# Optimization experiments

Hardware: AMD Instinct MI355X
Metric: run time of the kernel (lower is better)

Reference implementation:

```python
import jax, jax.numpy as jnp
import numpy as np

T, H, I, E, Z, TOPK = 1024, 1024, 512, 32, 8, 4
ROUTED_SCALING = 1.0


def setup_inputs() -> dict:
    key = jax.random.key(0)
    k1, k2, k3, k4 = jax.random.split(key, 4)
    return {
        "hidden_states": jax.random.normal(k1, (T, H), jnp.float32),
        "router_w": jax.random.normal(k2, (E + Z, H), jnp.float32) * 0.02,
        "correction_bias": jnp.zeros((E + Z,), jnp.float32),
        "w_gate_up": jax.random.normal(k3, (E, 2 * I, H), jnp.float32) * 0.02,
        "w_down": jax.random.normal(k4, (E, H, I), jnp.float32) * 0.02,
        "top_k": TOPK,
    }


def reference(hidden_states, router_w, correction_bias, w_gate_up, w_down, top_k):
    # hidden_states: [T, H]; router_w: [E+Z, H]; w_gate_up: [E, 2I, H]; w_down: [E, H, I]
    t, h = hidden_states.shape
    e = w_gate_up.shape[0]
    i = w_down.shape[2]
    # --- router (float32, no bias; correction bias only affects selection) ---
    logits = jnp.einsum("th,eh->te", hidden_states.astype(jnp.float32), router_w)
    scores = jax.nn.softmax(logits, axis=-1)                     # [T, E+Z]
    _, idx = jax.lax.top_k(scores + correction_bias[None, :], top_k)  # [T, k]
    w = jnp.take_along_axis(scores, idx, axis=1) * ROUTED_SCALING     # renormalize=False
    # combine matrix [T, E+Z] (sparse top-k scattered dense)
    comb = jnp.zeros((t, scores.shape[1]), jnp.float32)
    comb = comb.at[jnp.arange(t)[:, None], idx].add(w)
    comb_routed = comb[:, :e].astype(hidden_states.dtype)        # [T, E]
    zero_w = comb[:, e:].sum(-1).astype(hidden_states.dtype)     # [T] identity zero-experts
    # --- grouped SiLU-gated expert MLPs (dense all-experts reference) ---
    gu = jnp.einsum("th,eih->eti", hidden_states, w_gate_up)     # [E, T, 2I]
    hmid = jax.nn.silu(gu[..., :i]) * gu[..., i:]                # [E, T, I]
    ye = jnp.einsum("eti,ehi->eth", hmid, w_down)                # [E, T, H]
    out = jnp.einsum("te,eth->th", comb_routed, ye)
    out = out + zero_w[:, None] * hidden_states
    return out
```

## Files before the change

### kernel.cpp

```cpp
#include <hip/hip_runtime.h>
#include <hip/hip_cooperative_groups.h>
#include <hip/hip_bf16.h>
#include <math.h>

namespace cg = cooperative_groups;

#define TT   1024
#define HH   1024
#define II   512
#define EE   32
#define NE   40
#define TOPK 4
#define CAP  1024

#define GM  128
#define GNP 32
#define GK  32
#define KP  40
#define DN  64

typedef __attribute__((ext_vector_type(4))) short short4v;
typedef __attribute__((ext_vector_type(8))) short short8v;
typedef __attribute__((ext_vector_type(4))) float floatx4;

static __device__ __forceinline__ short f2bf(float f) {
    unsigned u = __float_as_uint(f);
    unsigned r = (u + 0x7fffu + ((u >> 16) & 1u)) >> 16;
    return (short)(r & 0xffffu);
}
static __device__ __forceinline__ float bf2f(short s) {
    return __uint_as_float(((unsigned)(unsigned short)s) << 16);
}
#if defined(__has_builtin)
#if __has_builtin(__builtin_amdgcn_cvt_pk_bf16_f32)
#define HAVE_PK_BF16 1
#endif
#endif
static __device__ __forceinline__ unsigned pk2(float a, float b) {
#ifdef HAVE_PK_BF16
    typedef __attribute__((ext_vector_type(2))) __bf16 bf2t;
    union { bf2t v; unsigned u; } cv;
    cv.v = __builtin_amdgcn_cvt_pk_bf16_f32(a, b);
    return cv.u;
#else
    return (unsigned)(unsigned short)f2bf(a) | ((unsigned)(unsigned short)f2bf(b) << 16);
#endif
}
static __device__ __forceinline__ short4v cvt4(float4 v) {
    union { unsigned u[2]; short4v s; } cv;
    cv.u[0] = pk2(v.x, v.y); cv.u[1] = pk2(v.z, v.w);
    return cv.s;
}

struct SMem {
    short As[GM * KP];
    short Bs[2 * GNP * KP];
    int   sl[GM];
    float wvs[GM];
};


static __device__ __forceinline__ void phaseA(
    const int bx, const int tid,
    const float* __restrict__ x, const float* __restrict__ rw,
    const float* __restrict__ bias,
    float* __restrict__ topk_w, float* __restrict__ zero_w,
    int* __restrict__ kexp, int* __restrict__ counts,
    int* __restrict__ slots, short* __restrict__ xb)
{
    const int lane = tid & 63;
    const int w    = tid >> 6;

    if (w < 2) {
        const int t = bx * 2 + w;
        float xv[16];
        #pragma unroll
        for (int i = 0; i < 16; ++i) xv[i] = x[(size_t)t * HH + 64 * i + lane];

        float mylogit = -INFINITY;
        for (int e0 = 0; e0 < NE; e0 += 4) {
            const float* r0 = rw + (size_t)e0 * HH;
            float p[4] = { 0.f, 0.f, 0.f, 0.f };
            #pragma unroll
            for (int i = 0; i < 16; ++i) {
                int h = 64 * i + lane;
                #pragma unroll
                for (int j = 0; j < 4; ++j) p[j] += xv[i] * r0[(size_t)j * HH + h];
            }
            #pragma unroll
            for (int j = 0; j < 4; ++j) {
                #pragma unroll
                for (int off = 32; off > 0; off >>= 1) p[j] += __shfl_xor(p[j], off);
                if (lane == e0 + j) mylogit = p[j];
            }
        }

        float m = mylogit;
        #pragma unroll
        for (int off = 32; off > 0; off >>= 1) m = fmaxf(m, __shfl_xor(m, off));
        float pexp = (lane < NE) ? expf(mylogit - m) : 0.f;
        float s = pexp;
        #pragma unroll
        for (int off = 32; off > 0; off >>= 1) s += __shfl_xor(s, off);
        const float score = pexp / s;

        float val = (lane < NE) ? score + bias[lane] : -INFINITY;
        int   kidx[TOPK];
        float kw[TOPK];
        #pragma unroll
        for (int k = 0; k < TOPK; ++k) {
            float v = val; int idx = lane;
            #pragma unroll
            for (int off = 32; off > 0; off >>= 1) {
                float ov = __shfl_xor(v, off);
                int   oi = __shfl_xor(idx, off);
                if (ov > v || (ov == v && oi < idx)) { v = ov; idx = oi; }
            }
            kidx[k] = idx;
            kw[k]   = __shfl(score, idx);
            if (lane == idx) val = -INFINITY;
        }

        if (lane == 0) {
            float zw = 0.f;
            #pragma unroll
            for (int k = 0; k < TOPK; ++k) {
                int slot = t * TOPK + k;
                topk_w[slot] = kw[k];
                kexp[slot]   = kidx[k];
                if (kidx[k] < EE) {
                    int pos = atomicAdd(&counts[kidx[k]], 1);
                    slots[kidx[k] * CAP + pos] = slot;
                } else {
                    zw += kw[k];
                }
            }
            zero_w[t] = zw;
        }
    } else {
        const int t = bx * 2 + (w - 2);
        const float4* xr = (const float4*)(x + (size_t)t * HH);
        short4v* xbr = (short4v*)(xb + (size_t)t * HH);
        #pragma unroll
        for (int i = 0; i < 4; ++i) xbr[lane + 64 * i] = cvt4(xr[lane + 64 * i]);
    }
}

static __device__ __forceinline__ void phaseB(
    const int bx, const int tid, SMem* sm,
    const short* __restrict__ xb, const float* __restrict__ wgu,
    const int* __restrict__ counts, const int* __restrict__ slots,
    const float* __restrict__ topk_w, short* __restrict__ hmid)
{
    const int e      = bx >> 4;
    const int c_base = (bx & 15) * GNP;
    const int cnt    = counts[e];
    const float* wb  = wgu + (size_t)e * (2 * II) * HH;

    const int lane = tid & 63;
    const int w    = tid >> 6;
    const int wy   = w & 1;
    const int wx   = w >> 1;
    const int quad = lane >> 4;
    const int mcol = lane & 15;

    for (int m_base = 0; m_base < cnt; m_base += GM) {
        if (tid < GM) {
            int m = m_base + tid;
            int s = (m < cnt) ? slots[e * CAP + m] : -1;
            sm->sl[tid]  = s;
            sm->wvs[tid] = (s >= 0) ? topk_w[s] : 0.f;
        }
        __syncthreads();

        const int kcA = tid & 3;
        int rowA[2]; int slA[2]; const short* pA[2];
        #pragma unroll
        for (int it = 0; it < 2; ++it) {
            rowA[it] = (tid >> 2) + 64 * it;
            int s = sm->sl[rowA[it]];
            slA[it] = s;
            pA[it] = xb + (size_t)((s >= 0 ? s : 0) >> 2) * HH + kcA * 8;
        }
        const int kq = tid & 7;
        int rowB[2]; const float* pB[2];
        #pragma unroll
        for (int it = 0; it < 2; ++it) {
            rowB[it] = (tid >> 3) + 32 * it;
            int grow = (rowB[it] < GNP) ? (c_base + rowB[it])
                                        : (II + c_base + rowB[it] - GNP);
            pB[it] = wb + (size_t)grow * HH + kq * 4;
        }

        floatx4 accg[4] = {};
        floatx4 accu[4] = {};
        short8v pa[2]; float4 pb[2];
        const short8v szv = { 0,0,0,0,0,0,0,0 };

        #pragma unroll
        for (int it = 0; it < 2; ++it) pa[it] = (slA[it] >= 0) ? *(const short8v*)(pA[it]) : szv;
        #pragma unroll
        for (int it = 0; it < 2; ++it) pb[it] = *(const float4*)(pB[it]);

        for (int k0 = 0; k0 < HH; k0 += GK) {
            #pragma unroll
            for (int it = 0; it < 2; ++it) *(short8v*)&sm->As[rowA[it] * KP + kcA * 8] = pa[it];
            #pragma unroll
            for (int it = 0; it < 2; ++it) *(short4v*)&sm->Bs[rowB[it] * KP + kq * 4] = cvt4(pb[it]);
            __syncthreads();

            const int kn = k0 + GK;
            if (kn < HH) {
                #pragma unroll
                for (int it = 0; it < 2; ++it) pa[it] = (slA[it] >= 0) ? *(const short8v*)(pA[it] + kn) : szv;
                #pragma unroll
                for (int it = 0; it < 2; ++it) pb[it] = *(const float4*)(pB[it] + kn);
            }

            short8v a[4], bg, bu;
            #pragma unroll
            for (int i = 0; i < 4; ++i)
                a[i] = *(const short8v*)&sm->As[(wy * 64 + i * 16 + mcol) * KP + quad * 8];
            bg = *(const short8v*)&sm->Bs[(wx * 16 + mcol) * KP + quad * 8];
            bu = *(const short8v*)&sm->Bs[(GNP + wx * 16 + mcol) * KP + quad * 8];
            #pragma unroll
            for (int i = 0; i < 4; ++i) {
                accg[i] = __builtin_amdgcn_mfma_f32_16x16x32_bf16(a[i], bg, accg[i], 0, 0, 0);
                accu[i] = __builtin_amdgcn_mfma_f32_16x16x32_bf16(a[i], bu, accu[i], 0, 0, 0);
            }
            __syncthreads();
        }

        #pragma unroll
        for (int i = 0; i < 4; ++i) {
            #pragma unroll
            for (int r = 0; r < 4; ++r) {
                int m = wy * 64 + i * 16 + quad * 4 + r;
                int s = sm->sl[m];
                if (s < 0) continue;
                float g = accg[i][r], u = accu[i][r];
                float valf = sm->wvs[m] * g * u / (1.f + __expf(-g));
                hmid[(size_t)s * II + c_base + wx * 16 + mcol] = f2bf(valf);
            }
        }
        __syncthreads();
    }
}

static __device__ __forceinline__ void phaseC(
    const int bx, const int tid, SMem* sm,
    const short* __restrict__ hmid, const float* __restrict__ wd,
    const int* __restrict__ counts, const int* __restrict__ slots,
    short* __restrict__ ydown)
{
    const int e      = bx >> 4;
    const int n_base = (bx & 15) * DN;
    const int cnt    = counts[e];
    const float* wb  = wd + (size_t)e * HH * II;

    const int lane = tid & 63;
    const int w    = tid >> 6;
    const int wy   = w & 1;
    const int wx   = w >> 1;
    const int quad = lane >> 4;
    const int mcol = lane & 15;

    for (int m_base = 0; m_base < cnt; m_base += GM) {
        if (tid < GM) {
            int m = m_base + tid;
            sm->sl[tid] = (m < cnt) ? slots[e * CAP + m] : -1;
        }
        __syncthreads();

        const int kcA = tid & 3;
        int rowA[2]; int slA[2]; const short* pA[2];
        #pragma unroll
        for (int it = 0; it < 2; ++it) {
            rowA[it] = (tid >> 2) + 64 * it;
            int s = sm->sl[rowA[it]];
            slA[it] = s;
            pA[it] = hmid + (size_t)(s >= 0 ? s : 0) * II + kcA * 8;
        }
        const int kq = tid & 7;
        int rowB[2]; const float* pB[2];
        #pragma unroll
        for (int it = 0; it < 2; ++it) {
            rowB[it] = (tid >> 3) + 32 * it;
            pB[it] = wb + (size_t)(n_base + rowB[it]) * II + kq * 4;
        }

        floatx4 acc[4][2] = {};
        short8v pa[2]; float4 pb[2];
        const short8v szv = { 0,0,0,0,0,0,0,0 };

        #pragma unroll
        for (int it = 0; it < 2; ++it) pa[it] = (slA[it] >= 0) ? *(const short8v*)(pA[it]) : szv;
        #pragma unroll
        for (int it = 0; it < 2; ++it) pb[it] = *(const float4*)(pB[it]);

        for (int k0 = 0; k0 < II; k0 += GK) {
            #pragma unroll
            for (int it = 0; it < 2; ++it) *(short8v*)&sm->As[rowA[it] * KP + kcA * 8] = pa[it];
            #pragma unroll
            for (int it = 0; it < 2; ++it) *(short4v*)&sm->Bs[rowB[it] * KP + kq * 4] = cvt4(pb[it]);
            __syncthreads();

            const int kn = k0 + GK;
            if (kn < II) {
                #pragma unroll
                for (int it = 0; it < 2; ++it) pa[it] = (slA[it] >= 0) ? *(const short8v*)(pA[it] + kn) : szv;
                #pragma unroll
                for (int it = 0; it < 2; ++it) pb[it] = *(const float4*)(pB[it] + kn);
            }

            short8v a[4], b[2];
            #pragma unroll
            for (int i = 0; i < 4; ++i)
                a[i] = *(const short8v*)&sm->As[(wy * 64 + i * 16 + mcol) * KP + quad * 8];
            #pragma unroll
            for (int j = 0; j < 2; ++j)
                b[j] = *(const short8v*)&sm->Bs[(wx * 32 + j * 16 + mcol) * KP + quad * 8];
            #pragma unroll
            for (int i = 0; i < 4; ++i)
                #pragma unroll
                for (int j = 0; j < 2; ++j)
                    acc[i][j] = __builtin_amdgcn_mfma_f32_16x16x32_bf16(a[i], b[j], acc[i][j], 0, 0, 0);
            __syncthreads();
        }

        #pragma unroll
        for (int i = 0; i < 4; ++i) {
            #pragma unroll
            for (int r = 0; r < 4; ++r) {
                int m = wy * 64 + i * 16 + quad * 4 + r;
                int s = sm->sl[m];
                if (s < 0) continue;
                short* yrow = ydown + (size_t)s * HH + n_base + wx * 32;
                #pragma unroll
                for (int j = 0; j < 2; ++j)
                    yrow[j * 16 + mcol] = f2bf(acc[i][j][r]);
            }
        }
        __syncthreads();
    }
}

static __device__ __forceinline__ void phaseD(
    const int bx, const int tid,
    const float* __restrict__ x, const short* __restrict__ ydown,
    const int* __restrict__ kexp, const float* __restrict__ zero_w,
    float* __restrict__ out)
{
    #pragma unroll
    for (int j = 0; j < 2; ++j) {
        const int t = bx * 2 + j;
        const float4 xvv = ((const float4*)(x + (size_t)t * HH))[tid];
        const float zw = zero_w[t];
        float4 o;
        o.x = zw * xvv.x; o.y = zw * xvv.y; o.z = zw * xvv.z; o.w = zw * xvv.w;
        #pragma unroll
        for (int k = 0; k < TOPK; ++k) {
            int slot = t * TOPK + k;
            if (kexp[slot] < EE) {
                short4v y = *(const short4v*)&ydown[(size_t)slot * HH + tid * 4];
                o.x += bf2f(y[0]); o.y += bf2f(y[1]);
                o.z += bf2f(y[2]); o.w += bf2f(y[3]);
            }
        }
        ((float4*)(out + (size_t)t * HH))[tid] = o;
    }
}

__global__ __launch_bounds__(256, 2) void fused_moe(
    const float* __restrict__ x, const float* __restrict__ rw,
    const float* __restrict__ bias, const float* __restrict__ wgu,
    const float* __restrict__ wd, float* __restrict__ out,
    int* __restrict__ counts, float* __restrict__ topk_w,
    float* __restrict__ zero_w, int* __restrict__ kexp,
    int* __restrict__ slots, short* __restrict__ xb,
    short* __restrict__ hmid, short* __restrict__ ydown)
{
    cg::grid_group grid = cg::this_grid();
    __shared__ SMem sm;
    const int bx = blockIdx.x, tid = threadIdx.x;

    phaseA(bx, tid, x, rw, bias, topk_w, zero_w, kexp, counts, slots, xb);
    __threadfence(); grid.sync();
    phaseB(bx, tid, &sm, xb, wgu, counts, slots, topk_w, hmid);
    __threadfence(); grid.sync();
    phaseC(bx, tid, &sm, hmid, wd, counts, slots, ydown);
    __threadfence(); grid.sync();
    phaseD(bx, tid, x, ydown, kexp, zero_w, out);
}

__global__ __launch_bounds__(256, 2) void kA(
    const float* __restrict__ x, const float* __restrict__ rw,
    const float* __restrict__ bias, float* __restrict__ topk_w,
    float* __restrict__ zero_w, int* __restrict__ kexp,
    int* __restrict__ counts, int* __restrict__ slots, short* __restrict__ xb)
{
    phaseA(blockIdx.x, threadIdx.x, x, rw, bias, topk_w, zero_w, kexp, counts, slots, xb);
}
__global__ __launch_bounds__(256, 2) void kB(
    const short* __restrict__ xb, const float* __restrict__ wgu,
    const int* __restrict__ counts, const int* __restrict__ slots,
    const float* __restrict__ topk_w, short* __restrict__ hmid)
{
    __shared__ SMem sm;
    phaseB(blockIdx.x, threadIdx.x, &sm, xb, wgu, counts, slots, topk_w, hmid);
}
__global__ __launch_bounds__(256, 2) void kC(
    const short* __restrict__ hmid, const float* __restrict__ wd,
    const int* __restrict__ counts, const int* __restrict__ slots,
    short* __restrict__ ydown)
{
    __shared__ SMem sm;
    phaseC(blockIdx.x, threadIdx.x, &sm, hmid, wd, counts, slots, ydown);
}
__global__ __launch_bounds__(256, 2) void kD(
    const float* __restrict__ x, const short* __restrict__ ydown,
    const int* __restrict__ kexp, const float* __restrict__ zero_w,
    float* __restrict__ out)
{
    phaseD(blockIdx.x, threadIdx.x, x, ydown, kexp, zero_w, out);
}

extern "C" void kernel_launch(void* const* d_in, const int* in_sizes, int n_in,
                              void* d_out, int out_size, void* d_ws, size_t ws_size,
                              hipStream_t stream) {
    const float* x    = (const float*)d_in[0];
    const float* rw   = (const float*)d_in[1];
    const float* bias = (const float*)d_in[2];
    const float* wgu  = (const float*)d_in[3];
    const float* wd   = (const float*)d_in[4];
    float* out = (float*)d_out;

    char* ws = (char*)d_ws;
    int*   counts = (int*)ws;
    float* topk_w = (float*)(ws + 1024);
    float* zero_w = (float*)(ws + 17408);
    int*   kexp   = (int*)(ws + 21504);
    int*   slots  = (int*)(ws + 40960);
    short* xb     = (short*)(ws + 262144);
    short* hmid   = (short*)(ws + 2359296);
    short* ydown  = (short*)(ws + 6553600);

    hipMemsetAsync(counts, 0, EE * sizeof(int), stream);

    int nb = 0;
    hipError_t qerr = hipOccupancyMaxActiveBlocksPerMultiprocessor(&nb, fused_moe, 256, 0);
    bool launched = false;
    if (qerr == hipSuccess && nb >= 2) {
        void* args[] = {
            (void*)&x, (void*)&rw, (void*)&bias, (void*)&wgu, (void*)&wd,
            (void*)&out, (void*)&counts, (void*)&topk_w, (void*)&zero_w,
            (void*)&kexp, (void*)&slots, (void*)&xb, (void*)&hmid, (void*)&ydown
        };
        hipError_t lerr = hipLaunchCooperativeKernel((const void*)fused_moe,
                                                     dim3(512), dim3(256),
                                                     args, 0, stream);
        launched = (lerr == hipSuccess);
    }
    if (!launched) {
        kA<<<dim3(512), dim3(256), 0, stream>>>(x, rw, bias, topk_w, zero_w, kexp, counts, slots, xb);
        kB<<<dim3(512), dim3(256), 0, stream>>>(xb, wgu, counts, slots, topk_w, hmid);
        kC<<<dim3(512), dim3(256), 0, stream>>>(hmid, wd, counts, slots, ydown);
        kD<<<dim3(512), dim3(256), 0, stream>>>(x, ydown, kexp, zero_w, out);
    }
}
```

Before: 311.7 us.

## Replace cooperative fused kernel with four launches using smaller tiles

Removes the cooperative single-kernel path with grid syncs and always launches four separate kernels. Tile widths for the gate/up and down GEMMs are halved so each expert gets 32 blocks, giving 1024 blocks per GEMM, and each warp now owns 32 rows. Launch bounds rise to 4 blocks per CU and the combine kernel uses one block per token. The aim is more parallelism and occupancy and no grid-wide barriers, at the cost of extra launch overhead and more redundant reads of the activation rows per expert.

```diff
diff --git a/kernel.cpp b/kernel.cpp
--- a/kernel.cpp
+++ b/kernel.cpp
@@ -1,9 +1,6 @@
 #include <hip/hip_runtime.h>
-#include <hip/hip_cooperative_groups.h>
 #include <hip/hip_bf16.h>
 #include <math.h>
-
-namespace cg = cooperative_groups;
 
 #define TT   1024
 #define HH   1024
@@ -14,10 +11,10 @@
 #define CAP  1024
 
 #define GM  128
-#define GNP 32
+#define GNP 16
 #define GK  32
 #define KP  40
-#define DN  64
+#define DN  32
 
 typedef __attribute__((ext_vector_type(4))) short short4v;
 typedef __attribute__((ext_vector_type(8))) short short8v;
@@ -60,14 +57,13 @@
 };
 
 
-static __device__ __forceinline__ void phaseA(
-    const int bx, const int tid,
+__global__ __launch_bounds__(256, 4) void kA(
     const float* __restrict__ x, const float* __restrict__ rw,
-    const float* __restrict__ bias,
-    float* __restrict__ topk_w, float* __restrict__ zero_w,
-    int* __restrict__ kexp, int* __restrict__ counts,
-    int* __restrict__ slots, short* __restrict__ xb)
+    const float* __restrict__ bias, float* __restrict__ topk_w,
+    float* __restrict__ zero_w, int* __restrict__ kexp,
+    int* __restrict__ counts, int* __restrict__ slots, short* __restrict__ xb)
 {
+    const int bx = blockIdx.x, tid = threadIdx.x;
     const int lane = tid & 63;
     const int w    = tid >> 6;
 
@@ -146,283 +142,210 @@
     }
 }
 
-static __device__ __forceinline__ void phaseB(
-    const int bx, const int tid, SMem* sm,
-    const short* __restrict__ xb, const float* __restrict__ wgu,
-    const int* __restrict__ counts, const int* __restrict__ slots,
-    const float* __restrict__ topk_w, short* __restrict__ hmid)
-{
-    const int e      = bx >> 4;
-    const int c_base = (bx & 15) * GNP;
-    const int cnt    = counts[e];
-    const float* wb  = wgu + (size_t)e * (2 * II) * HH;
-
-    const int lane = tid & 63;
-    const int w    = tid >> 6;
-    const int wy   = w & 1;
-    const int wx   = w >> 1;
-    const int quad = lane >> 4;
-    const int mcol = lane & 15;
-
-    for (int m_base = 0; m_base < cnt; m_base += GM) {
-        if (tid < GM) {
-            int m = m_base + tid;
-            int s = (m < cnt) ? slots[e * CAP + m] : -1;
-            sm->sl[tid]  = s;
-            sm->wvs[tid] = (s >= 0) ? topk_w[s] : 0.f;
-        }
-        __syncthreads();
-
-        const int kcA = tid & 3;
-        int rowA[2]; int slA[2]; const short* pA[2];
-        #pragma unroll
-        for (int it = 0; it < 2; ++it) {
-            rowA[it] = (tid >> 2) + 64 * it;
-            int s = sm->sl[rowA[it]];
-            slA[it] = s;
-            pA[it] = xb + (size_t)((s >= 0 ? s : 0) >> 2) * HH + kcA * 8;
-        }
-        const int kq = tid & 7;
-        int rowB[2]; const float* pB[2];
-        #pragma unroll
-        for (int it = 0; it < 2; ++it) {
-            rowB[it] = (tid >> 3) + 32 * it;
-            int grow = (rowB[it] < GNP) ? (c_base + rowB[it])
-                                        : (II + c_base + rowB[it] - GNP);
-            pB[it] = wb + (size_t)grow * HH + kq * 4;
-        }
-
-        floatx4 accg[4] = {};
-        floatx4 accu[4] = {};
-        short8v pa[2]; float4 pb[2];
-        const short8v szv = { 0,0,0,0,0,0,0,0 };
-
-        #pragma unroll
-        for (int it = 0; it < 2; ++it) pa[it] = (slA[it] >= 0) ? *(const short8v*)(pA[it]) : szv;
-        #pragma unroll
-        for (int it = 0; it < 2; ++it) pb[it] = *(const float4*)(pB[it]);
-
-        for (int k0 = 0; k0 < HH; k0 += GK) {
-            #pragma unroll
-            for (int it = 0; it < 2; ++it) *(short8v*)&sm->As[rowA[it] * KP + kcA * 8] = pa[it];
-            #pragma unroll
-            for (int it = 0; it < 2; ++it) *(short4v*)&sm->Bs[rowB[it] * KP + kq * 4] = cvt4(pb[it]);
-            __syncthreads();
-
-            const int kn = k0 + GK;
-            if (kn < HH) {
-                #pragma unroll
-                for (int it = 0; it < 2; ++it) pa[it] = (slA[it] >= 0) ? *(const short8v*)(pA[it] + kn) : szv;
-                #pragma unroll
-                for (int it = 0; it < 2; ++it) pb[it] = *(const float4*)(pB[it] + kn);
-            }
-
-            short8v a[4], bg, bu;
-            #pragma unroll
-            for (int i = 0; i < 4; ++i)
-                a[i] = *(const short8v*)&sm->As[(wy * 64 + i * 16 + mcol) * KP + quad * 8];
-            bg = *(const short8v*)&sm->Bs[(wx * 16 + mcol) * KP + quad * 8];
-            bu = *(const short8v*)&sm->Bs[(GNP + wx * 16 + mcol) * KP + quad * 8];
-            #pragma unroll
-            for (int i = 0; i < 4; ++i) {
-                accg[i] = __builtin_amdgcn_mfma_f32_16x16x32_bf16(a[i], bg, accg[i], 0, 0, 0);
-                accu[i] = __builtin_amdgcn_mfma_f32_16x16x32_bf16(a[i], bu, accu[i], 0, 0, 0);
-            }
-            __syncthreads();
-        }
-
-        #pragma unroll
-        for (int i = 0; i < 4; ++i) {
-            #pragma unroll
-            for (int r = 0; r < 4; ++r) {
-                int m = wy * 64 + i * 16 + quad * 4 + r;
-                int s = sm->sl[m];
-                if (s < 0) continue;
-                float g = accg[i][r], u = accu[i][r];
-                float valf = sm->wvs[m] * g * u / (1.f + __expf(-g));
-                hmid[(size_t)s * II + c_base + wx * 16 + mcol] = f2bf(valf);
-            }
-        }
-        __syncthreads();
-    }
-}
-
-static __device__ __forceinline__ void phaseC(
-    const int bx, const int tid, SMem* sm,
-    const short* __restrict__ hmid, const float* __restrict__ wd,
-    const int* __restrict__ counts, const int* __restrict__ slots,
-    short* __restrict__ ydown)
-{
-    const int e      = bx >> 4;
-    const int n_base = (bx & 15) * DN;
-    const int cnt    = counts[e];
-    const float* wb  = wd + (size_t)e * HH * II;
-
-    const int lane = tid & 63;
-    const int w    = tid >> 6;
-    const int wy   = w & 1;
-    const int wx   = w >> 1;
-    const int quad = lane >> 4;
-    const int mcol = lane & 15;
-
-    for (int m_base = 0; m_base < cnt; m_base += GM) {
-        if (tid < GM) {
-            int m = m_base + tid;
-            sm->sl[tid] = (m < cnt) ? slots[e * CAP + m] : -1;
-        }
-        __syncthreads();
-
-        const int kcA = tid & 3;
-        int rowA[2]; int slA[2]; const short* pA[2];
-        #pragma unroll
-        for (int it = 0; it < 2; ++it) {
-            rowA[it] = (tid >> 2) + 64 * it;
-            int s = sm->sl[rowA[it]];
-            slA[it] = s;
-            pA[it] = hmid + (size_t)(s >= 0 ? s : 0) * II + kcA * 8;
-        }
-        const int kq = tid & 7;
-        int rowB[2]; const float* pB[2];
-        #pragma unroll
-        for (int it = 0; it < 2; ++it) {
-            rowB[it] = (tid >> 3) + 32 * it;
-            pB[it] = wb + (size_t)(n_base + rowB[it]) * II + kq * 4;
-        }
-
-        floatx4 acc[4][2] = {};
-        short8v pa[2]; float4 pb[2];
-        const short8v szv = { 0,0,0,0,0,0,0,0 };
-
-        #pragma unroll
-        for (int it = 0; it < 2; ++it) pa[it] = (slA[it] >= 0) ? *(const short8v*)(pA[it]) : szv;
-        #pragma unroll
-        for (int it = 0; it < 2; ++it) pb[it] = *(const float4*)(pB[it]);
-
-        for (int k0 = 0; k0 < II; k0 += GK) {
-            #pragma unroll
-            for (int it = 0; it < 2; ++it) *(short8v*)&sm->As[rowA[it] * KP + kcA * 8] = pa[it];
-            #pragma unroll
-            for (int it = 0; it < 2; ++it) *(short4v*)&sm->Bs[rowB[it] * KP + kq * 4] = cvt4(pb[it]);
-            __syncthreads();
-
-            const int kn = k0 + GK;
-            if (kn < II) {
-                #pragma unroll
-                for (int it = 0; it < 2; ++it) pa[it] = (slA[it] >= 0) ? *(const short8v*)(pA[it] + kn) : szv;
-                #pragma unroll
-                for (int it = 0; it < 2; ++it) pb[it] = *(const float4*)(pB[it] + kn);
-            }
-
-            short8v a[4], b[2];
-            #pragma unroll
-            for (int i = 0; i < 4; ++i)
-                a[i] = *(const short8v*)&sm->As[(wy * 64 + i * 16 + mcol) * KP + quad * 8];
-            #pragma unroll
-            for (int j = 0; j < 2; ++j)
-                b[j] = *(const short8v*)&sm->Bs[(wx * 32 + j * 16 + mcol) * KP + quad * 8];
-            #pragma unroll
-            for (int i = 0; i < 4; ++i)
-                #pragma unroll
-                for (int j = 0; j < 2; ++j)
-                    acc[i][j] = __builtin_amdgcn_mfma_f32_16x16x32_bf16(a[i], b[j], acc[i][j], 0, 0, 0);
-            __syncthreads();
-        }
-
-        #pragma unroll
-        for (int i = 0; i < 4; ++i) {
-            #pragma unroll
-            for (int r = 0; r < 4; ++r) {
-                int m = wy * 64 + i * 16 + quad * 4 + r;
-                int s = sm->sl[m];
-                if (s < 0) continue;
-                short* yrow = ydown + (size_t)s * HH + n_base + wx * 32;
-                #pragma unroll
-                for (int j = 0; j < 2; ++j)
-                    yrow[j * 16 + mcol] = f2bf(acc[i][j][r]);
-            }
-        }
-        __syncthreads();
-    }
-}
-
-static __device__ __forceinline__ void phaseD(
-    const int bx, const int tid,
-    const float* __restrict__ x, const short* __restrict__ ydown,
-    const int* __restrict__ kexp, const float* __restrict__ zero_w,
-    float* __restrict__ out)
-{
-    #pragma unroll
-    for (int j = 0; j < 2; ++j) {
-        const int t = bx * 2 + j;
-        const float4 xvv = ((const float4*)(x + (size_t)t * HH))[tid];
-        const float zw = zero_w[t];
-        float4 o;
-        o.x = zw * xvv.x; o.y = zw * xvv.y; o.z = zw * xvv.z; o.w = zw * xvv.w;
-        #pragma unroll
-        for (int k = 0; k < TOPK; ++k) {
-            int slot = t * TOPK + k;
-            if (kexp[slot] < EE) {
-                short4v y = *(const short4v*)&ydown[(size_t)slot * HH + tid * 4];
-                o.x += bf2f(y[0]); o.y += bf2f(y[1]);
-                o.z += bf2f(y[2]); o.w += bf2f(y[3]);
-            }
-        }
-        ((float4*)(out + (size_t)t * HH))[tid] = o;
-    }
-}
-
-__global__ __launch_bounds__(256, 2) void fused_moe(
-    const float* __restrict__ x, const float* __restrict__ rw,
-    const float* __restrict__ bias, const float* __restrict__ wgu,
-    const float* __restrict__ wd, float* __restrict__ out,
-    int* __restrict__ counts, float* __restrict__ topk_w,
-    float* __restrict__ zero_w, int* __restrict__ kexp,
-    int* __restrict__ slots, short* __restrict__ xb,
-    short* __restrict__ hmid, short* __restrict__ ydown)
-{
-    cg::grid_group grid = cg::this_grid();
-    __shared__ SMem sm;
-    const int bx = blockIdx.x, tid = threadIdx.x;
-
-    phaseA(bx, tid, x, rw, bias, topk_w, zero_w, kexp, counts, slots, xb);
-    __threadfence(); grid.sync();
-    phaseB(bx, tid, &sm, xb, wgu, counts, slots, topk_w, hmid);
-    __threadfence(); grid.sync();
-    phaseC(bx, tid, &sm, hmid, wd, counts, slots, ydown);
-    __threadfence(); grid.sync();
-    phaseD(bx, tid, x, ydown, kexp, zero_w, out);
-}
-
-__global__ __launch_bounds__(256, 2) void kA(
-    const float* __restrict__ x, const float* __restrict__ rw,
-    const float* __restrict__ bias, float* __restrict__ topk_w,
-    float* __restrict__ zero_w, int* __restrict__ kexp,
-    int* __restrict__ counts, int* __restrict__ slots, short* __restrict__ xb)
-{
-    phaseA(blockIdx.x, threadIdx.x, x, rw, bias, topk_w, zero_w, kexp, counts, slots, xb);
-}
-__global__ __launch_bounds__(256, 2) void kB(
+__global__ __launch_bounds__(256, 4) void kB(
     const short* __restrict__ xb, const float* __restrict__ wgu,
     const int* __restrict__ counts, const int* __restrict__ slots,
     const float* __restrict__ topk_w, short* __restrict__ hmid)
 {
     __shared__ SMem sm;
-    phaseB(blockIdx.x, threadIdx.x, &sm, xb, wgu, counts, slots, topk_w, hmid);
-}
-__global__ __launch_bounds__(256, 2) void kC(
+    const int bx = blockIdx.x, tid = threadIdx.x;
+    const int e      = bx >> 5;
+    const int c_base = (bx & 31) * GNP;
+    const int cnt    = counts[e];
+    const float* wb  = wgu + (size_t)e * (2 * II) * HH;
+
+    const int lane = tid & 63;
+    const int w    = tid >> 6;
+    const int quad = lane >> 4;
+    const int mcol = lane & 15;
+
+    for (int m_base = 0; m_base < cnt; m_base += GM) {
+        if (tid < GM) {
+            int m = m_base + tid;
+            int s = (m < cnt) ? slots[e * CAP + m] : -1;
+            sm.sl[tid]  = s;
+            sm.wvs[tid] = (s >= 0) ? topk_w[s] : 0.f;
+        }
+        __syncthreads();
+
+        const int kcA = tid & 3;
+        int rowA[2]; int slA[2]; const short* pA[2];
+        #pragma unroll
+        for (int it = 0; it < 2; ++it) {
+            rowA[it] = (tid >> 2) + 64 * it;
+            int s = sm.sl[rowA[it]];
+            slA[it] = s;
+            pA[it] = xb + (size_t)((s >= 0 ? s : 0) >> 2) * HH + kcA * 8;
+        }
+        const int kq   = tid & 7;
+        const int rowB = tid >> 3;
+        const int grow = (rowB < GNP) ? (c_base + rowB)
+                                      : (II + c_base + (rowB - GNP));
+        const float* pB = wb + (size_t)grow * HH + kq * 4;
+
+        floatx4 accg[2] = {};
+        floatx4 accu[2] = {};
+        short8v pa[2]; float4 pb;
+        const short8v szv = { 0,0,0,0,0,0,0,0 };
+
+        #pragma unroll
+        for (int it = 0; it < 2; ++it) pa[it] = (slA[it] >= 0) ? *(const short8v*)(pA[it]) : szv;
+        pb = *(const float4*)(pB);
+
+        for (int k0 = 0; k0 < HH; k0 += GK) {
+            #pragma unroll
+            for (int it = 0; it < 2; ++it) *(short8v*)&sm.As[rowA[it] * KP + kcA * 8] = pa[it];
+            *(short4v*)&sm.Bs[rowB * KP + kq * 4] = cvt4(pb);
+            __syncthreads();
+
+            const int kn = k0 + GK;
+            if (kn < HH) {
+                #pragma unroll
+                for (int it = 0; it < 2; ++it) pa[it] = (slA[it] >= 0) ? *(const short8v*)(pA[it] + kn) : szv;
+                pb = *(const float4*)(pB + kn);
+            }
+
+            short8v a[2], bg, bu;
+            #pragma unroll
+            for (int i = 0; i < 2; ++i)
+                a[i] = *(const short8v*)&sm.As[(w * 32 + i * 16 + mcol) * KP + quad * 8];
+            bg = *(const short8v*)&sm.Bs[(mcol) * KP + quad * 8];
+            bu = *(const short8v*)&sm.Bs[(GNP + mcol) * KP + quad * 8];
+            #pragma unroll
+            for (int i = 0; i < 2; ++i) {
+                accg[i] = __builtin_amdgcn_mfma_f32_16x16x32_bf16(a[i], bg, accg[i], 0, 0, 0);
+                accu[i] = __builtin_amdgcn_mfma_f32_16x16x32_bf16(a[i], bu, accu[i], 0, 0, 0);
+            }
+            __syncthreads();
+        }
+
+        #pragma unroll
+        for (int i = 0; i < 2; ++i) {
+            #pragma unroll
+            for (int r = 0; r < 4; ++r) {
+                int m = w * 32 + i * 16 + quad * 4 + r;
+                int s = sm.sl[m];
+                if (s < 0) continue;
+                float g = accg[i][r], u = accu[i][r];
+                float valf = sm.wvs[m] * g * u / (1.f + __expf(-g));
+                hmid[(size_t)s * II + c_base + mcol] = f2bf(valf);
+            }
+        }
+        __syncthreads();
+    }
+}
+
+__global__ __launch_bounds__(256, 4) void kC(
     const short* __restrict__ hmid, const float* __restrict__ wd,
     const int* __restrict__ counts, const int* __restrict__ slots,
     short* __restrict__ ydown)
 {
     __shared__ SMem sm;
-    phaseC(blockIdx.x, threadIdx.x, &sm, hmid, wd, counts, slots, ydown);
-}
-__global__ __launch_bounds__(256, 2) void kD(
+    const int bx = blockIdx.x, tid = threadIdx.x;
+    const int e      = bx >> 5;
+    const int n_base = (bx & 31) * DN;
+    const int cnt    = counts[e];
+    const float* wb  = wd + (size_t)e * HH * II;
+
+    const int lane = tid & 63;
+    const int w    = tid >> 6;
+    const int quad = lane >> 4;
+    const int mcol = lane & 15;
+
+    for (int m_base = 0; m_base < cnt; m_base += GM) {
+        if (tid < GM) {
+            int m = m_base + tid;
+            sm.sl[tid] = (m < cnt) ? slots[e * CAP + m] : -1;
+        }
+        __syncthreads();
+
+        const int kcA = tid & 3;
+        int rowA[2]; int slA[2]; const short* pA[2];
+        #pragma unroll
+        for (int it = 0; it < 2; ++it) {
+            rowA[it] = (tid >> 2) + 64 * it;
+            int s = sm.sl[rowA[it]];
+            slA[it] = s;
+            pA[it] = hmid + (size_t)(s >= 0 ? s : 0) * II + kcA * 8;
+        }
+        const int kq   = tid & 7;
+        const int rowB = tid >> 3;
+        const float* pB = wb + (size_t)(n_base + rowB) * II + kq * 4;
+
+        floatx4 acc[2][2] = {};
+        short8v pa[2]; float4 pb;
+        const short8v szv = { 0,0,0,0,0,0,0,0 };
+
+        #pragma unroll
+        for (int it = 0; it < 2; ++it) pa[it] = (slA[it] >= 0) ? *(const short8v*)(pA[it]) : szv;
+        pb = *(const float4*)(pB);
+
+        for (int k0 = 0; k0 < II; k0 += GK) {
+            #pragma unroll
+            for (int it = 0; it < 2; ++it) *(short8v*)&sm.As[rowA[it] * KP + kcA * 8] = pa[it];
+            *(short4v*)&sm.Bs[rowB * KP + kq * 4] = cvt4(pb);
+            __syncthreads();
+
+            const int kn = k0 + GK;
+            if (kn < II) {
+                #pragma unroll
+                for (int it = 0; it < 2; ++it) pa[it] = (slA[it] >= 0) ? *(const short8v*)(pA[it] + kn) : szv;
+                pb = *(const float4*)(pB + kn);
+            }
+
+            short8v a[2], b[2];
+            #pragma unroll
+            for (int i = 0; i < 2; ++i)
+                a[i] = *(const short8v*)&sm.As[(w * 32 + i * 16 + mcol) * KP + quad * 8];
+            #pragma unroll
+            for (int j = 0; j < 2; ++j)
+                b[j] = *(const short8v*)&sm.Bs[(j * 16 + mcol) * KP + quad * 8];
+            #pragma unroll
+            for (int i = 0; i < 2; ++i)
+                #pragma unroll
+                for (int j = 0; j < 2; ++j)
+                    acc[i][j] = __builtin_amdgcn_mfma_f32_16x16x32_bf16(a[i], b[j], acc[i][j], 0, 0, 0);
+            __syncthreads();
+        }
+
+        #pragma unroll
+        for (int i = 0; i < 2; ++i) {
+            #pragma unroll
+            for (int r = 0; r < 4; ++r) {
+                int m = w * 32 + i * 16 + quad * 4 + r;
+                int s = sm.sl[m];
+                if (s < 0) continue;
+                short* yrow = ydown + (size_t)s * HH + n_base;
+                #pragma unroll
+                for (int j = 0; j < 2; ++j)
+                    yrow[j * 16 + mcol] = f2bf(acc[i][j][r]);
+            }
+        }
+        __syncthreads();
+    }
+}
+
+__global__ __launch_bounds__(256, 4) void kD(
     const float* __restrict__ x, const short* __restrict__ ydown,
     const int* __restrict__ kexp, const float* __restrict__ zero_w,
     float* __restrict__ out)
 {
-    phaseD(blockIdx.x, threadIdx.x, x, ydown, kexp, zero_w, out);
+    const int bx = blockIdx.x, tid = threadIdx.x;
+    const int t = bx;
+    const float4 xvv = ((const float4*)(x + (size_t)t * HH))[tid];
+    const float zw = zero_w[t];
+    float4 o;
+    o.x = zw * xvv.x; o.y = zw * xvv.y; o.z = zw * xvv.z; o.w = zw * xvv.w;
+    #pragma unroll
+    for (int k = 0; k < TOPK; ++k) {
+        int slot = t * TOPK + k;
+        if (kexp[slot] < EE) {
+            short4v y = *(const short4v*)&ydown[(size_t)slot * HH + tid * 4];
+            o.x += bf2f(y[0]); o.y += bf2f(y[1]);
+            o.z += bf2f(y[2]); o.w += bf2f(y[3]);
+        }
+    }
+    ((float4*)(out + (size_t)t * HH))[tid] = o;
 }
 
 extern "C" void kernel_launch(void* const* d_in, const int* in_sizes, int n_in,
@@ -447,24 +370,8 @@
 
     hipMemsetAsync(counts, 0, EE * sizeof(int), stream);
 
-    int nb = 0;
-    hipError_t qerr = hipOccupancyMaxActiveBlocksPerMultiprocessor(&nb, fused_moe, 256, 0);
-    bool launched = false;
-    if (qerr == hipSuccess && nb >= 2) {
-        void* args[] = {
-            (void*)&x, (void*)&rw, (void*)&bias, (void*)&wgu, (void*)&wd,
-            (void*)&out, (void*)&counts, (void*)&topk_w, (void*)&zero_w,
-            (void*)&kexp, (void*)&slots, (void*)&xb, (void*)&hmid, (void*)&ydown
-        };
-        hipError_t lerr = hipLaunchCooperativeKernel((const void*)fused_moe,
-                                                     dim3(512), dim3(256),
-                                                     args, 0, stream);
-        launched = (lerr == hipSuccess);
-    }
-    if (!launched) {
-        kA<<<dim3(512), dim3(256), 0, stream>>>(x, rw, bias, topk_w, zero_w, kexp, counts, slots, xb);
-        kB<<<dim3(512), dim3(256), 0, stream>>>(xb, wgu, counts, slots, topk_w, hmid);
-        kC<<<dim3(512), dim3(256), 0, stream>>>(hmid, wd, counts, slots, ydown);
-        kD<<<dim3(512), dim3(256), 0, stream>>>(x, ydown, kexp, zero_w, out);
-    }
-}
+    kA<<<dim3(512),  dim3(256), 0, stream>>>(x, rw, bias, topk_w, zero_w, kexp, counts, slots, xb);
+    kB<<<dim3(1024), dim3(256), 0, stream>>>(xb, wgu, counts, slots, topk_w, hmid);
+    kC<<<dim3(1024), dim3(256), 0, stream>>>(hmid, wd, counts, slots, ydown);
+    kD<<<dim3(1024), dim3(256), 0, stream>>>(x, ydown, kexp, zero_w, out);
+}
```

Result: slower. 319.6 us (+2.5%).
